# Kernel tuning notes

Measured on AMD Instinct MI355X. Metric: run time of the kernel, lower is better.

Reference implementation:

```python
import jax, jax.numpy as jnp
import numpy as np

N_RES = 262144
C_S = 384
C_H = 128   # num_channels
N_BINS = 50


def setup_inputs() -> dict:
    key = jax.random.key(0)
    ks = jax.random.split(key, 9)
    s = lambda fan_in: 1.0 / np.sqrt(fan_in)
    return {
        "x": jax.random.normal(ks[0], (N_RES, C_S), dtype=jnp.float32),
        "ln_scale": jnp.ones((C_S,), dtype=jnp.float32),
        "ln_bias": jnp.zeros((C_S,), dtype=jnp.float32),
        "w0": jax.random.uniform(ks[1], (C_S, C_H), jnp.float32, -s(C_S), s(C_S)),
        "b0": jax.random.uniform(ks[2], (C_H,), jnp.float32, -s(C_S), s(C_S)),
        "w1": jax.random.uniform(ks[3], (C_H, C_H), jnp.float32, -s(C_H), s(C_H)),
        "b1": jax.random.uniform(ks[4], (C_H,), jnp.float32, -s(C_H), s(C_H)),
        "w2": jax.random.uniform(ks[5], (C_H, N_BINS), jnp.float32, -s(C_H), s(C_H)),
        "b2": jax.random.uniform(ks[6], (N_BINS,), jnp.float32, -s(C_H), s(C_H)),
    }


def _layer_norm(x, scale, bias, eps=1e-5):
    mu = jnp.mean(x, axis=-1, keepdims=True)
    var = jnp.mean(jnp.square(x - mu), axis=-1, keepdims=True)
    return (x - mu) * jax.lax.rsqrt(var + eps) * scale + bias


def reference(x, ln_scale, ln_bias, w0, b0, w1, b1, w2, b2):
    act = _layer_norm(x, ln_scale, ln_bias)            # [N_res, 384]
    act = jax.nn.relu(act @ w0 + b0)                   # [N_res, 128]
    act = jax.nn.relu(act @ w1 + b1)                   # [N_res, 128]
    logits = act @ w2 + b2                             # [N_res, 50]
    return logits
```

## Files before the change

kernel.cpp:

```cpp
#include <hip/hip_runtime.h>

typedef short bf16x8 __attribute__((ext_vector_type(8)));
typedef float f32x4 __attribute__((ext_vector_type(4)));

#define NRES 262144
#define BM 32
#define GOODMAGIC 0x600DF00Du

#define WT0H 0
#define WT0L 49152
#define WT1H 98304
#define WT1L 114688
#define WT2H 131072
#define WT2L 139264
#define PREP_N 73728
#define WS_NEED ((size_t)(16 + PREP_N * 2 * 2))

#define A0H 0
#define A0L 12544
#define AC0H 25088
#define AC0L 29440
#define A1H 0
#define A1L 12544
#define SMU 33792
#define A0_STR 392
#define ACT_STR 136

__device__ __forceinline__ unsigned short f2bf(float f) {
    unsigned u = __builtin_bit_cast(unsigned, f);
    u += 0x7FFFu + ((u >> 16) & 1u);
    return (unsigned short)(u >> 16);
}
__device__ __forceinline__ float bf2f(unsigned short h) {
    unsigned u = ((unsigned)h) << 16;
    return __builtin_bit_cast(float, u);
}

__global__ void set_flag(unsigned* flag, unsigned v) {
    if (threadIdx.x == 0 && blockIdx.x == 0) *flag = v;
}

__device__ __forceinline__ void prep_index(int i, const float* w0, const float* w1,
                                           const float* w2, float& v, int& hi_off, int& lo_off) {
    if (i < 49152) {
        int col = i / 384, k = i % 384;
        v = w0[k * 128 + col]; hi_off = WT0H + i; lo_off = WT0L + i;
    } else if (i < 65536) {
        int j = i - 49152; int col = j / 128, k = j % 128;
        v = w1[k * 128 + col]; hi_off = WT1H + j; lo_off = WT1L + j;
    } else {
        int j = i - 65536; int col = j / 128, k = j % 128;
        v = (col < 50) ? w2[k * 50 + col] : 0.0f; hi_off = WT2H + j; lo_off = WT2L + j;
    }
}

__global__ void prep_weights(const float* __restrict__ w0, const float* __restrict__ w1,
                             const float* __restrict__ w2, unsigned short* __restrict__ wt) {
    const int i = blockIdx.x * blockDim.x + threadIdx.x;
    if (i >= PREP_N) return;
    float v; int hi_off, lo_off;
    prep_index(i, w0, w1, w2, v, hi_off, lo_off);
    const unsigned short h = f2bf(v);
    wt[hi_off] = h;
    wt[lo_off] = f2bf(v - bf2f(h));
}

__global__ void check_weights(const float* __restrict__ w0, const float* __restrict__ w1,
                              const float* __restrict__ w2, const unsigned short* __restrict__ wt,
                              unsigned* flag) {
    const int i = blockIdx.x * blockDim.x + threadIdx.x;
    if (i >= PREP_N) return;
    float v; int hi_off, lo_off;
    prep_index(i, w0, w1, w2, v, hi_off, lo_off);
    const unsigned short h = f2bf(v);
    const unsigned short l = f2bf(v - bf2f(h));
    if (wt[hi_off] != h || wt[lo_off] != l) atomicExch(flag, 0xBAD0BAD0u);
}

__device__ __forceinline__ void ln_phase(const float* __restrict__ x,
                                         const float* __restrict__ ln_scale,
                                         const float* __restrict__ ln_bias,
                                         unsigned short* sm, int tid, long rowBase) {
    const float4* x4 = (const float4*)x;
    const int j = tid & 15;
#pragma unroll
    for (int rep = 0; rep < 2; ++rep) {
        const int row = rep * 16 + (tid >> 4);
        const long gr = rowBase + row;
        float4 v[6];
#pragma unroll
        for (int cs = 0; cs < 6; ++cs)
            v[cs] = x4[gr * 96 + cs * 16 + j];

        float s = 0.f, sq = 0.f;
#pragma unroll
        for (int cs = 0; cs < 6; ++cs) {
            s  += v[cs].x + v[cs].y + v[cs].z + v[cs].w;
            sq += v[cs].x*v[cs].x + v[cs].y*v[cs].y + v[cs].z*v[cs].z + v[cs].w*v[cs].w;
        }
#pragma unroll
        for (int d = 1; d < 16; d <<= 1) {
            s  += __shfl_xor(s,  d);
            sq += __shfl_xor(sq, d);
        }
        const float mu  = s * (1.0f / 384.0f);
        const float var = sq * (1.0f / 384.0f) - mu * mu;
        const float rs  = rsqrtf(var + 1e-5f);
#pragma unroll
        for (int cs = 0; cs < 6; ++cs) {
            const float4 sc = ((const float4*)ln_scale)[cs * 16 + j];
            const float4 bi = ((const float4*)ln_bias )[cs * 16 + j];
            float f[4];
            f[0] = (v[cs].x - mu) * rs * sc.x + bi.x;
            f[1] = (v[cs].y - mu) * rs * sc.y + bi.y;
            f[2] = (v[cs].z - mu) * rs * sc.z + bi.z;
            f[3] = (v[cs].w - mu) * rs * sc.w + bi.w;
            union { unsigned short h[4]; uint2 u; } ph, pl;
#pragma unroll
            for (int e = 0; e < 4; ++e) {
                ph.h[e] = f2bf(f[e]);
                pl.h[e] = f2bf(f[e] - bf2f(ph.h[e]));
            }
            const int idx = row * A0_STR + cs * 64 + j * 4;
            *(uint2*)&sm[A0H + idx] = ph.u;
            *(uint2*)&sm[A0L + idx] = pl.u;
        }
    }
}

__global__ __launch_bounds__(256, 2)
void lddt_ws(const float* __restrict__ x,
             const float* __restrict__ ln_scale,
             const float* __restrict__ ln_bias,
             const unsigned short* __restrict__ wt,
             const unsigned* __restrict__ flag,
             const float* __restrict__ b0,
             const float* __restrict__ b1,
             const float* __restrict__ b2,
             float* __restrict__ out) {
    if (*flag != GOODMAGIC) return;

    __shared__ __align__(16) unsigned short sm[SMU];
    const int tid  = threadIdx.x;
    const int lane = tid & 63;
    const int l15  = lane & 15;
    const int lg   = lane >> 4;
    const int wid  = tid >> 6;
    const long rowBase = (long)blockIdx.x * BM;

    ln_phase(x, ln_scale, ln_bias, sm, tid, rowBase);
    __syncthreads();

    {
        f32x4 acc[2][2];
#pragma unroll
        for (int m = 0; m < 2; ++m) { acc[m][0] = (f32x4)0.0f; acc[m][1] = (f32x4)0.0f; }
#pragma unroll
        for (int s = 0; s < 12; ++s) {
            bf16x8 bh[2], bl[2], ah[2], al[2];
#pragma unroll
            for (int n = 0; n < 2; ++n) {
                const int bcol = wid * 32 + n * 16 + l15;
                bh[n] = *(const bf16x8*)&wt[WT0H + bcol * 384 + s * 32 + lg * 8];
                bl[n] = *(const bf16x8*)&wt[WT0L + bcol * 384 + s * 32 + lg * 8];
            }
#pragma unroll
            for (int m = 0; m < 2; ++m) {
                const int idx = (m * 16 + l15) * A0_STR + s * 32 + lg * 8;
                ah[m] = *(const bf16x8*)&sm[A0H + idx];
                al[m] = *(const bf16x8*)&sm[A0L + idx];
            }
#pragma unroll
            for (int m = 0; m < 2; ++m)
#pragma unroll
                for (int n = 0; n < 2; ++n) {
                    acc[m][n] = __builtin_amdgcn_mfma_f32_16x16x32_bf16(ah[m], bh[n], acc[m][n], 0, 0, 0);
                    acc[m][n] = __builtin_amdgcn_mfma_f32_16x16x32_bf16(ah[m], bl[n], acc[m][n], 0, 0, 0);
                    acc[m][n] = __builtin_amdgcn_mfma_f32_16x16x32_bf16(al[m], bh[n], acc[m][n], 0, 0, 0);
                }
        }
#pragma unroll
        for (int m = 0; m < 2; ++m)
#pragma unroll
            for (int n = 0; n < 2; ++n) {
                const int col = wid * 32 + n * 16 + l15;
                const float bb = b0[col];
#pragma unroll
                for (int r = 0; r < 4; ++r) {
                    const int row = m * 16 + lg * 4 + r;
                    const float z = fmaxf(acc[m][n][r] + bb, 0.0f);
                    const unsigned short h = f2bf(z);
                    const int idx = row * ACT_STR + col;
                    sm[AC0H + idx] = h;
                    sm[AC0L + idx] = f2bf(z - bf2f(h));
                }
            }
    }
    __syncthreads();

    {
        f32x4 acc[2][2];
#pragma unroll
        for (int m = 0; m < 2; ++m) { acc[m][0] = (f32x4)0.0f; acc[m][1] = (f32x4)0.0f; }
#pragma unroll
        for (int s = 0; s < 4; ++s) {
            bf16x8 bh[2], bl[2], ah[2], al[2];
#pragma unroll
            for (int n = 0; n < 2; ++n) {
                const int bcol = wid * 32 + n * 16 + l15;
                bh[n] = *(const bf16x8*)&wt[WT1H + bcol * 128 + s * 32 + lg * 8];
                bl[n] = *(const bf16x8*)&wt[WT1L + bcol * 128 + s * 32 + lg * 8];
            }
#pragma unroll
            for (int m = 0; m < 2; ++m) {
                const int idx = (m * 16 + l15) * ACT_STR + s * 32 + lg * 8;
                ah[m] = *(const bf16x8*)&sm[AC0H + idx];
                al[m] = *(const bf16x8*)&sm[AC0L + idx];
            }
#pragma unroll
            for (int m = 0; m < 2; ++m)
#pragma unroll
                for (int n = 0; n < 2; ++n) {
                    acc[m][n] = __builtin_amdgcn_mfma_f32_16x16x32_bf16(ah[m], bh[n], acc[m][n], 0, 0, 0);
                    acc[m][n] = __builtin_amdgcn_mfma_f32_16x16x32_bf16(ah[m], bl[n], acc[m][n], 0, 0, 0);
                    acc[m][n] = __builtin_amdgcn_mfma_f32_16x16x32_bf16(al[m], bh[n], acc[m][n], 0, 0, 0);
                }
        }
#pragma unroll
        for (int m = 0; m < 2; ++m)
#pragma unroll
            for (int n = 0; n < 2; ++n) {
                const int col = wid * 32 + n * 16 + l15;
                const float bb = b1[col];
#pragma unroll
                for (int r = 0; r < 4; ++r) {
                    const int row = m * 16 + lg * 4 + r;
                    const float z = fmaxf(acc[m][n][r] + bb, 0.0f);
                    const unsigned short h = f2bf(z);
                    const int idx = row * ACT_STR + col;
                    sm[A1H + idx] = h;
                    sm[A1L + idx] = f2bf(z - bf2f(h));
                }
            }
    }
    __syncthreads();

    {
        f32x4 acc[2];
        acc[0] = (f32x4)0.0f; acc[1] = (f32x4)0.0f;
        const int bcol = wid * 16 + l15;
#pragma unroll
        for (int s = 0; s < 4; ++s) {
            bf16x8 bh, bl, ah[2], al[2];
            bh = *(const bf16x8*)&wt[WT2H + bcol * 128 + s * 32 + lg * 8];
            bl = *(const bf16x8*)&wt[WT2L + bcol * 128 + s * 32 + lg * 8];
#pragma unroll
            for (int m = 0; m < 2; ++m) {
                const int idx = (m * 16 + l15) * ACT_STR + s * 32 + lg * 8;
                ah[m] = *(const bf16x8*)&sm[A1H + idx];
                al[m] = *(const bf16x8*)&sm[A1L + idx];
            }
#pragma unroll
            for (int m = 0; m < 2; ++m) {
                acc[m] = __builtin_amdgcn_mfma_f32_16x16x32_bf16(ah[m], bh, acc[m], 0, 0, 0);
                acc[m] = __builtin_amdgcn_mfma_f32_16x16x32_bf16(ah[m], bl, acc[m], 0, 0, 0);
                acc[m] = __builtin_amdgcn_mfma_f32_16x16x32_bf16(al[m], bh, acc[m], 0, 0, 0);
            }
        }
        if (bcol < 50) {
            const float bb = b2[bcol];
#pragma unroll
            for (int m = 0; m < 2; ++m)
#pragma unroll
                for (int r = 0; r < 4; ++r) {
                    const long row = rowBase + m * 16 + lg * 4 + r;
                    out[row * 50 + bcol] = acc[m][r] + bb;
                }
        }
    }
}

__device__ __forceinline__ void bfrag(const float* __restrict__ w, int ldw, int col, int k0,
                                      bf16x8& bh, bf16x8& bl) {
    union { unsigned u[4]; bf16x8 v; } H, L;
#pragma unroll
    for (int jj = 0; jj < 4; ++jj) {
        const float f0 = w[(k0 + 2 * jj)     * ldw + col];
        const float f1 = w[(k0 + 2 * jj + 1) * ldw + col];
        const unsigned short h0 = f2bf(f0), h1 = f2bf(f1);
        const unsigned short l0 = f2bf(f0 - bf2f(h0)), l1 = f2bf(f1 - bf2f(h1));
        H.u[jj] = (unsigned)h0 | ((unsigned)h1 << 16);
        L.u[jj] = (unsigned)l0 | ((unsigned)l1 << 16);
    }
    bh = H.v; bl = L.v;
}
__device__ __forceinline__ void bfrag50(const float* __restrict__ w, int col, int k0,
                                        bf16x8& bh, bf16x8& bl) {
    union { unsigned u[4]; bf16x8 v; } H, L;
    const bool ok = (col < 50);
#pragma unroll
    for (int jj = 0; jj < 4; ++jj) {
        const float f0 = ok ? w[(k0 + 2 * jj)     * 50 + col] : 0.0f;
        const float f1 = ok ? w[(k0 + 2 * jj + 1) * 50 + col] : 0.0f;
        const unsigned short h0 = f2bf(f0), h1 = f2bf(f1);
        const unsigned short l0 = f2bf(f0 - bf2f(h0)), l1 = f2bf(f1 - bf2f(h1));
        H.u[jj] = (unsigned)h0 | ((unsigned)h1 << 16);
        L.u[jj] = (unsigned)l0 | ((unsigned)l1 << 16);
    }
    bh = H.v; bl = L.v;
}

__global__ __launch_bounds__(256, 2)
void lddt_conv(const float* __restrict__ x,
               const float* __restrict__ ln_scale,
               const float* __restrict__ ln_bias,
               const float* __restrict__ w0,
               const float* __restrict__ b0,
               const float* __restrict__ w1,
               const float* __restrict__ b1,
               const float* __restrict__ w2,
               const float* __restrict__ b2,
               const unsigned* flag,
               float* __restrict__ out) {
    if (flag && *flag == GOODMAGIC) return;

    __shared__ __align__(16) unsigned short sm[SMU];
    const int tid  = threadIdx.x;
    const int lane = tid & 63;
    const int l15  = lane & 15;
    const int lg   = lane >> 4;
    const int wid  = tid >> 6;
    const long rowBase = (long)blockIdx.x * BM;

    ln_phase(x, ln_scale, ln_bias, sm, tid, rowBase);
    __syncthreads();

    {
        f32x4 acc[2][2];
#pragma unroll
        for (int m = 0; m < 2; ++m) { acc[m][0] = (f32x4)0.0f; acc[m][1] = (f32x4)0.0f; }
#pragma unroll
        for (int s = 0; s < 12; ++s) {
            bf16x8 bh[2], bl[2], ah[2], al[2];
#pragma unroll
            for (int n = 0; n < 2; ++n)
                bfrag(w0, 128, wid * 32 + n * 16 + l15, s * 32 + lg * 8, bh[n], bl[n]);
#pragma unroll
            for (int m = 0; m < 2; ++m) {
                const int idx = (m * 16 + l15) * A0_STR + s * 32 + lg * 8;
                ah[m] = *(const bf16x8*)&sm[A0H + idx];
                al[m] = *(const bf16x8*)&sm[A0L + idx];
            }
#pragma unroll
            for (int m = 0; m < 2; ++m)
#pragma unroll
                for (int n = 0; n < 2; ++n) {
                    acc[m][n] = __builtin_amdgcn_mfma_f32_16x16x32_bf16(ah[m], bh[n], acc[m][n], 0, 0, 0);
                    acc[m][n] = __builtin_amdgcn_mfma_f32_16x16x32_bf16(ah[m], bl[n], acc[m][n], 0, 0, 0);
                    acc[m][n] = __builtin_amdgcn_mfma_f32_16x16x32_bf16(al[m], bh[n], acc[m][n], 0, 0, 0);
                }
        }
#pragma unroll
        for (int m = 0; m < 2; ++m)
#pragma unroll
            for (int n = 0; n < 2; ++n) {
                const int col = wid * 32 + n * 16 + l15;
                const float bb = b0[col];
#pragma unroll
                for (int r = 0; r < 4; ++r) {
                    const int row = m * 16 + lg * 4 + r;
                    const float z = fmaxf(acc[m][n][r] + bb, 0.0f);
                    const unsigned short h = f2bf(z);
                    const int idx = row * ACT_STR + col;
                    sm[AC0H + idx] = h;
                    sm[AC0L + idx] = f2bf(z - bf2f(h));
                }
            }
    }
    __syncthreads();

    {
        f32x4 acc[2][2];
#pragma unroll
        for (int m = 0; m < 2; ++m) { acc[m][0] = (f32x4)0.0f; acc[m][1] = (f32x4)0.0f; }
#pragma unroll
        for (int s = 0; s < 4; ++s) {
            bf16x8 bh[2], bl[2], ah[2], al[2];
#pragma unroll
            for (int n = 0; n < 2; ++n)
                bfrag(w1, 128, wid * 32 + n * 16 + l15, s * 32 + lg * 8, bh[n], bl[n]);
#pragma unroll
            for (int m = 0; m < 2; ++m) {
                const int idx = (m * 16 + l15) * ACT_STR + s * 32 + lg * 8;
                ah[m] = *(const bf16x8*)&sm[AC0H + idx];
                al[m] = *(const bf16x8*)&sm[AC0L + idx];
            }
#pragma unroll
            for (int m = 0; m < 2; ++m)
#pragma unroll
                for (int n = 0; n < 2; ++n) {
                    acc[m][n] = __builtin_amdgcn_mfma_f32_16x16x32_bf16(ah[m], bh[n], acc[m][n], 0, 0, 0);
                    acc[m][n] = __builtin_amdgcn_mfma_f32_16x16x32_bf16(ah[m], bl[n], acc[m][n], 0, 0, 0);
                    acc[m][n] = __builtin_amdgcn_mfma_f32_16x16x32_bf16(al[m], bh[n], acc[m][n], 0, 0, 0);
                }
        }
#pragma unroll
        for (int m = 0; m < 2; ++m)
#pragma unroll
            for (int n = 0; n < 2; ++n) {
                const int col = wid * 32 + n * 16 + l15;
                const float bb = b1[col];
#pragma unroll
                for (int r = 0; r < 4; ++r) {
                    const int row = m * 16 + lg * 4 + r;
                    const float z = fmaxf(acc[m][n][r] + bb, 0.0f);
                    const unsigned short h = f2bf(z);
                    const int idx = row * ACT_STR + col;
                    sm[A1H + idx] = h;
                    sm[A1L + idx] = f2bf(z - bf2f(h));
                }
            }
    }
    __syncthreads();

    {
        f32x4 acc[2];
        acc[0] = (f32x4)0.0f; acc[1] = (f32x4)0.0f;
        const int bcol = wid * 16 + l15;
#pragma unroll
        for (int s = 0; s < 4; ++s) {
            bf16x8 bh, bl, ah[2], al[2];
            bfrag50(w2, bcol, s * 32 + lg * 8, bh, bl);
#pragma unroll
            for (int m = 0; m < 2; ++m) {
                const int idx = (m * 16 + l15) * ACT_STR + s * 32 + lg * 8;
                ah[m] = *(const bf16x8*)&sm[A1H + idx];
                al[m] = *(const bf16x8*)&sm[A1L + idx];
            }
#pragma unroll
            for (int m = 0; m < 2; ++m) {
                acc[m] = __builtin_amdgcn_mfma_f32_16x16x32_bf16(ah[m], bh, acc[m], 0, 0, 0);
                acc[m] = __builtin_amdgcn_mfma_f32_16x16x32_bf16(ah[m], bl, acc[m], 0, 0, 0);
                acc[m] = __builtin_amdgcn_mfma_f32_16x16x32_bf16(al[m], bh, acc[m], 0, 0, 0);
            }
        }
        if (bcol < 50) {
            const float bb = b2[bcol];
#pragma unroll
            for (int m = 0; m < 2; ++m)
#pragma unroll
                for (int r = 0; r < 4; ++r) {
                    const long row = rowBase + m * 16 + lg * 4 + r;
                    out[row * 50 + bcol] = acc[m][r] + bb;
                }
        }
    }
}

extern "C" void kernel_launch(void* const* d_in, const int* in_sizes, int n_in,
                              void* d_out, int out_size, void* d_ws, size_t ws_size,
                              hipStream_t stream) {
    const float* x        = (const float*)d_in[0];
    const float* ln_scale = (const float*)d_in[1];
    const float* ln_bias  = (const float*)d_in[2];
    const float* w0       = (const float*)d_in[3];
    const float* b0       = (const float*)d_in[4];
    const float* w1       = (const float*)d_in[5];
    const float* b1       = (const float*)d_in[6];
    const float* w2       = (const float*)d_in[7];
    const float* b2       = (const float*)d_in[8];
    float* out = (float*)d_out;

    const bool ws_ok = (ws_size >= WS_NEED);
    if (ws_ok) {
        unsigned* flag = (unsigned*)d_ws;
        unsigned short* wt = (unsigned short*)d_ws + 8;
        set_flag<<<1, 64, 0, stream>>>(flag, GOODMAGIC);
        prep_weights<<<(PREP_N + 255) / 256, 256, 0, stream>>>(w0, w1, w2, wt);
        check_weights<<<(PREP_N + 255) / 256, 256, 0, stream>>>(w0, w1, w2, wt, flag);
        lddt_ws<<<NRES / BM, 256, 0, stream>>>(
            x, ln_scale, ln_bias, wt, flag, b0, b1, b2, out);
        lddt_conv<<<NRES / BM, 256, 0, stream>>>(
            x, ln_scale, ln_bias, w0, b0, w1, b1, w2, b2, flag, out);
    } else {
        lddt_conv<<<NRES / BM, 256, 0, stream>>>(
            x, ln_scale, ln_bias, w0, b0, w1, b1, w2, b2, (const unsigned*)nullptr, out);
    }
}
```

Baseline: 347.5 us.

## Halve LayerNorm LDS tile by staging second K-half in registers for occupancy

The normalized input tile is split into two K halves. Only the first half goes to shared memory, while the second half's bf16 hi/lo pieces stay in registers until the first six GEMM slabs are done, then overwrite the same LDS region. This cuts shared memory per block from about 67KB to 43KB and raises launch bounds to 3 blocks per CU, aiming for more occupancy and latency hiding. In exchange it adds two extra barriers plus 24 held registers per thread, which may cause spills under the tighter register budget.

After: 383.4 us. 10.3% more time.

```diff
diff --git a/kernel.cpp b/kernel.cpp
--- a/kernel.cpp
+++ b/kernel.cpp
@@ -16,6 +16,16 @@
 #define PREP_N 73728
 #define WS_NEED ((size_t)(16 + PREP_N * 2 * 2))
 
+#define A0Hn 0
+#define A0Ln 6400
+#define AC0Hn 12800
+#define AC0Ln 17152
+#define A1Hn 0
+#define A1Ln 4352
+#define SMU2 21504
+#define A0_STR2 200
+#define ACT_STR 136
+
 #define A0H 0
 #define A0L 12544
 #define AC0H 25088
@@ -24,7 +34,6 @@
 #define A1L 12544
 #define SMU 33792
 #define A0_STR 392
-#define ACT_STR 136
 
 __device__ __forceinline__ unsigned short f2bf(float f) {
     unsigned u = __builtin_bit_cast(unsigned, f);
@@ -77,58 +86,7 @@
     if (wt[hi_off] != h || wt[lo_off] != l) atomicExch(flag, 0xBAD0BAD0u);
 }
 
-__device__ __forceinline__ void ln_phase(const float* __restrict__ x,
-                                         const float* __restrict__ ln_scale,
-                                         const float* __restrict__ ln_bias,
-                                         unsigned short* sm, int tid, long rowBase) {
-    const float4* x4 = (const float4*)x;
-    const int j = tid & 15;
-#pragma unroll
-    for (int rep = 0; rep < 2; ++rep) {
-        const int row = rep * 16 + (tid >> 4);
-        const long gr = rowBase + row;
-        float4 v[6];
-#pragma unroll
-        for (int cs = 0; cs < 6; ++cs)
-            v[cs] = x4[gr * 96 + cs * 16 + j];
-
-        float s = 0.f, sq = 0.f;
-#pragma unroll
-        for (int cs = 0; cs < 6; ++cs) {
-            s  += v[cs].x + v[cs].y + v[cs].z + v[cs].w;
-            sq += v[cs].x*v[cs].x + v[cs].y*v[cs].y + v[cs].z*v[cs].z + v[cs].w*v[cs].w;
-        }
-#pragma unroll
-        for (int d = 1; d < 16; d <<= 1) {
-            s  += __shfl_xor(s,  d);
-            sq += __shfl_xor(sq, d);
-        }
-        const float mu  = s * (1.0f / 384.0f);
-        const float var = sq * (1.0f / 384.0f) - mu * mu;
-        const float rs  = rsqrtf(var + 1e-5f);
-#pragma unroll
-        for (int cs = 0; cs < 6; ++cs) {
-            const float4 sc = ((const float4*)ln_scale)[cs * 16 + j];
-            const float4 bi = ((const float4*)ln_bias )[cs * 16 + j];
-            float f[4];
-            f[0] = (v[cs].x - mu) * rs * sc.x + bi.x;
-            f[1] = (v[cs].y - mu) * rs * sc.y + bi.y;
-            f[2] = (v[cs].z - mu) * rs * sc.z + bi.z;
-            f[3] = (v[cs].w - mu) * rs * sc.w + bi.w;
-            union { unsigned short h[4]; uint2 u; } ph, pl;
-#pragma unroll
-            for (int e = 0; e < 4; ++e) {
-                ph.h[e] = f2bf(f[e]);
-                pl.h[e] = f2bf(f[e] - bf2f(ph.h[e]));
-            }
-            const int idx = row * A0_STR + cs * 64 + j * 4;
-            *(uint2*)&sm[A0H + idx] = ph.u;
-            *(uint2*)&sm[A0L + idx] = pl.u;
-        }
-    }
-}
-
-__global__ __launch_bounds__(256, 2)
+__global__ __launch_bounds__(256, 3)
 void lddt_ws(const float* __restrict__ x,
              const float* __restrict__ ln_scale,
              const float* __restrict__ ln_bias,
@@ -140,7 +98,7 @@
              float* __restrict__ out) {
     if (*flag != GOODMAGIC) return;
 
-    __shared__ __align__(16) unsigned short sm[SMU];
+    __shared__ __align__(16) unsigned short sm[SMU2];
     const int tid  = threadIdx.x;
     const int lane = tid & 63;
     const int l15  = lane & 15;
@@ -148,37 +106,111 @@
     const int wid  = tid >> 6;
     const long rowBase = (long)blockIdx.x * BM;
 
-    ln_phase(x, ln_scale, ln_bias, sm, tid, rowBase);
+    uint2 h1s[2][3], l1s[2][3];
+    {
+        const float4* x4 = (const float4*)x;
+        const int j = tid & 15;
+#pragma unroll
+        for (int rep = 0; rep < 2; ++rep) {
+            const int row = rep * 16 + (tid >> 4);
+            const long gr = rowBase + row;
+            float4 v[6];
+#pragma unroll
+            for (int cs = 0; cs < 6; ++cs)
+                v[cs] = x4[gr * 96 + cs * 16 + j];
+
+            float s = 0.f, sq = 0.f;
+#pragma unroll
+            for (int cs = 0; cs < 6; ++cs) {
+                s  += v[cs].x + v[cs].y + v[cs].z + v[cs].w;
+                sq += v[cs].x*v[cs].x + v[cs].y*v[cs].y + v[cs].z*v[cs].z + v[cs].w*v[cs].w;
+            }
+#pragma unroll
+            for (int d = 1; d < 16; d <<= 1) {
+                s  += __shfl_xor(s,  d);
+                sq += __shfl_xor(sq, d);
+            }
+            const float mu  = s * (1.0f / 384.0f);
+            const float var = sq * (1.0f / 384.0f) - mu * mu;
+            const float rs  = rsqrtf(var + 1e-5f);
+#pragma unroll
+            for (int cs = 0; cs < 6; ++cs) {
+                const float4 sc = ((const float4*)ln_scale)[cs * 16 + j];
+                const float4 bi = ((const float4*)ln_bias )[cs * 16 + j];
+                float f[4];
+                f[0] = (v[cs].x - mu) * rs * sc.x + bi.x;
+                f[1] = (v[cs].y - mu) * rs * sc.y + bi.y;
+                f[2] = (v[cs].z - mu) * rs * sc.z + bi.z;
+                f[3] = (v[cs].w - mu) * rs * sc.w + bi.w;
+                union { unsigned short h[4]; uint2 u; } ph, pl;
+#pragma unroll
+                for (int e = 0; e < 4; ++e) {
+                    ph.h[e] = f2bf(f[e]);
+                    pl.h[e] = f2bf(f[e] - bf2f(ph.h[e]));
+                }
+                if (cs < 3) {
+                    const int idx = row * A0_STR2 + cs * 64 + j * 4;
+                    *(uint2*)&sm[A0Hn + idx] = ph.u;
+                    *(uint2*)&sm[A0Ln + idx] = pl.u;
+                } else {
+                    h1s[rep][cs - 3] = ph.u;
+                    l1s[rep][cs - 3] = pl.u;
+                }
+            }
+        }
+    }
     __syncthreads();
 
     {
         f32x4 acc[2][2];
 #pragma unroll
         for (int m = 0; m < 2; ++m) { acc[m][0] = (f32x4)0.0f; acc[m][1] = (f32x4)0.0f; }
-#pragma unroll
-        for (int s = 0; s < 12; ++s) {
-            bf16x8 bh[2], bl[2], ah[2], al[2];
-#pragma unroll
-            for (int n = 0; n < 2; ++n) {
-                const int bcol = wid * 32 + n * 16 + l15;
-                bh[n] = *(const bf16x8*)&wt[WT0H + bcol * 384 + s * 32 + lg * 8];
-                bl[n] = *(const bf16x8*)&wt[WT0L + bcol * 384 + s * 32 + lg * 8];
-            }
-#pragma unroll
-            for (int m = 0; m < 2; ++m) {
-                const int idx = (m * 16 + l15) * A0_STR + s * 32 + lg * 8;
-                ah[m] = *(const bf16x8*)&sm[A0H + idx];
-                al[m] = *(const bf16x8*)&sm[A0L + idx];
-            }
-#pragma unroll
-            for (int m = 0; m < 2; ++m)
-#pragma unroll
-                for (int n = 0; n < 2; ++n) {
-                    acc[m][n] = __builtin_amdgcn_mfma_f32_16x16x32_bf16(ah[m], bh[n], acc[m][n], 0, 0, 0);
-                    acc[m][n] = __builtin_amdgcn_mfma_f32_16x16x32_bf16(ah[m], bl[n], acc[m][n], 0, 0, 0);
-                    acc[m][n] = __builtin_amdgcn_mfma_f32_16x16x32_bf16(al[m], bh[n], acc[m][n], 0, 0, 0);
-                }
-        }
+
+#define G0SLAB(S, SL)                                                        \
+        {                                                                    \
+            bf16x8 bh[2], bl[2], ah[2], al[2];                               \
+            _Pragma("unroll")                                                \
+            for (int n = 0; n < 2; ++n) {                                    \
+                const int bcol = wid * 32 + n * 16 + l15;                    \
+                bh[n] = *(const bf16x8*)&wt[WT0H + bcol * 384 + (S) * 32 + lg * 8]; \
+                bl[n] = *(const bf16x8*)&wt[WT0L + bcol * 384 + (S) * 32 + lg * 8]; \
+            }                                                                \
+            _Pragma("unroll")                                                \
+            for (int m = 0; m < 2; ++m) {                                    \
+                const int idx = (m * 16 + l15) * A0_STR2 + (SL) * 32 + lg * 8; \
+                ah[m] = *(const bf16x8*)&sm[A0Hn + idx];                     \
+                al[m] = *(const bf16x8*)&sm[A0Ln + idx];                     \
+            }                                                                \
+            _Pragma("unroll")                                                \
+            for (int m = 0; m < 2; ++m)                                      \
+                _Pragma("unroll")                                            \
+                for (int n = 0; n < 2; ++n) {                                \
+                    acc[m][n] = __builtin_amdgcn_mfma_f32_16x16x32_bf16(ah[m], bh[n], acc[m][n], 0, 0, 0); \
+                    acc[m][n] = __builtin_amdgcn_mfma_f32_16x16x32_bf16(ah[m], bl[n], acc[m][n], 0, 0, 0); \
+                    acc[m][n] = __builtin_amdgcn_mfma_f32_16x16x32_bf16(al[m], bh[n], acc[m][n], 0, 0, 0); \
+                }                                                            \
+        }
+
+#pragma unroll
+        for (int s = 0; s < 6; ++s) G0SLAB(s, s)
+        __syncthreads();
+        {
+            const int j = tid & 15;
+#pragma unroll
+            for (int rep = 0; rep < 2; ++rep) {
+                const int row = rep * 16 + (tid >> 4);
+#pragma unroll
+                for (int c = 0; c < 3; ++c) {
+                    const int idx = row * A0_STR2 + c * 64 + j * 4;
+                    *(uint2*)&sm[A0Hn + idx] = h1s[rep][c];
+                    *(uint2*)&sm[A0Ln + idx] = l1s[rep][c];
+                }
+            }
+        }
+        __syncthreads();
+#pragma unroll
+        for (int s = 6; s < 12; ++s) G0SLAB(s, s - 6)
+
 #pragma unroll
         for (int m = 0; m < 2; ++m)
 #pragma unroll
@@ -191,8 +223,8 @@
                     const float z = fmaxf(acc[m][n][r] + bb, 0.0f);
                     const unsigned short h = f2bf(z);
                     const int idx = row * ACT_STR + col;
-                    sm[AC0H + idx] = h;
-                    sm[AC0L + idx] = f2bf(z - bf2f(h));
+                    sm[AC0Hn + idx] = h;
+                    sm[AC0Ln + idx] = f2bf(z - bf2f(h));
                 }
             }
     }
@@ -214,8 +246,8 @@
 #pragma unroll
             for (int m = 0; m < 2; ++m) {
                 const int idx = (m * 16 + l15) * ACT_STR + s * 32 + lg * 8;
-                ah[m] = *(const bf16x8*)&sm[AC0H + idx];
-                al[m] = *(const bf16x8*)&sm[AC0L + idx];
+                ah[m] = *(const bf16x8*)&sm[AC0Hn + idx];
+                al[m] = *(const bf16x8*)&sm[AC0Ln + idx];
             }
 #pragma unroll
             for (int m = 0; m < 2; ++m)
@@ -238,8 +270,8 @@
                     const float z = fmaxf(acc[m][n][r] + bb, 0.0f);
                     const unsigned short h = f2bf(z);
                     const int idx = row * ACT_STR + col;
-                    sm[A1H + idx] = h;
-                    sm[A1L + idx] = f2bf(z - bf2f(h));
+                    sm[A1Hn + idx] = h;
+                    sm[A1Ln + idx] = f2bf(z - bf2f(h));
                 }
             }
     }
@@ -257,8 +289,8 @@
 #pragma unroll
             for (int m = 0; m < 2; ++m) {
                 const int idx = (m * 16 + l15) * ACT_STR + s * 32 + lg * 8;
-                ah[m] = *(const bf16x8*)&sm[A1H + idx];
-                al[m] = *(const bf16x8*)&sm[A1L + idx];
+                ah[m] = *(const bf16x8*)&sm[A1Hn + idx];
+                al[m] = *(const bf16x8*)&sm[A1Ln + idx];
             }
 #pragma unroll
             for (int m = 0; m < 2; ++m) {
@@ -276,6 +308,57 @@
                     const long row = rowBase + m * 16 + lg * 4 + r;
                     out[row * 50 + bcol] = acc[m][r] + bb;
                 }
+        }
+    }
+}
+
+__device__ __forceinline__ void ln_phase(const float* __restrict__ x,
+                                         const float* __restrict__ ln_scale,
+                                         const float* __restrict__ ln_bias,
+                                         unsigned short* sm, int tid, long rowBase) {
+    const float4* x4 = (const float4*)x;
+    const int j = tid & 15;
+#pragma unroll
+    for (int rep = 0; rep < 2; ++rep) {
+        const int row = rep * 16 + (tid >> 4);
+        const long gr = rowBase + row;
+        float4 v[6];
+#pragma unroll
+        for (int cs = 0; cs < 6; ++cs)
+            v[cs] = x4[gr * 96 + cs * 16 + j];
+
+        float s = 0.f, sq = 0.f;
+#pragma unroll
+        for (int cs = 0; cs < 6; ++cs) {
+            s  += v[cs].x + v[cs].y + v[cs].z + v[cs].w;
+            sq += v[cs].x*v[cs].x + v[cs].y*v[cs].y + v[cs].z*v[cs].z + v[cs].w*v[cs].w;
+        }
+#pragma unroll
+        for (int d = 1; d < 16; d <<= 1) {
+            s  += __shfl_xor(s,  d);
+            sq += __shfl_xor(sq, d);
+        }
+        const float mu  = s * (1.0f / 384.0f);
+        const float var = sq * (1.0f / 384.0f) - mu * mu;
+        const float rs  = rsqrtf(var + 1e-5f);
+#pragma unroll
+        for (int cs = 0; cs < 6; ++cs) {
+            const float4 sc = ((const float4*)ln_scale)[cs * 16 + j];
+            const float4 bi = ((const float4*)ln_bias )[cs * 16 + j];
+            float f[4];
+            f[0] = (v[cs].x - mu) * rs * sc.x + bi.x;
+            f[1] = (v[cs].y - mu) * rs * sc.y + bi.y;
+            f[2] = (v[cs].z - mu) * rs * sc.z + bi.z;
+            f[3] = (v[cs].w - mu) * rs * sc.w + bi.w;
+            union { unsigned short h[4]; uint2 u; } ph, pl;
+#pragma unroll
+            for (int e = 0; e < 4; ++e) {
+                ph.h[e] = f2bf(f[e]);
+                pl.h[e] = f2bf(f[e] - bf2f(ph.h[e]));
+            }
+            const int idx = row * A0_STR + cs * 64 + j * 4;
+            *(uint2*)&sm[A0H + idx] = ph.u;
+            *(uint2*)&sm[A0L + idx] = pl.u;
         }
     }
 }
```
